# Kernel tuning notes

Measured on AMD Instinct MI355X. Metric: run time of the kernel, lower is better.

Reference implementation:

```python
import jax, jax.numpy as jnp
import numpy as np

ENC_IN, LAG = 14, 7
SEQ_LEN, PRED_LEN = 96, 96
NUM_SPLINE = 20
HID, LAYERS = 40, 2
F_RAW = ENC_IN + LAG - 1                 # 20 features into the CNN
F_CONV = F_RAW + 2 * 2 - (3 - 1) - 1 + 1 # 22 after Conv1d(k=3, pad=2)
F_CNN = (F_CONV + 2 * 1 - (3 - 1) - 1) // 2 + 1  # 11 after MaxPool1d(k=3, s=2, p=1)
B = 4096
T = SEQ_LEN + PRED_LEN                   # train_window = 192


def setup_inputs() -> dict:
    key = jax.random.key(0)
    ks = jax.random.split(key, 20)
    b0 = 0.02 * jax.random.normal(ks[10], (4 * HID,))
    b0 = b0.at[HID:2 * HID].add(2.0)  # forget-gate bias init (b_ih + b_hh = 1 + 1)
    b1 = 0.02 * jax.random.normal(ks[11], (4 * HID,))
    b1 = b1.at[HID:2 * HID].add(2.0)
    return {
        "x_enc": jax.random.normal(ks[0], (B, SEQ_LEN, ENC_IN + LAG), jnp.float32),
        "x_mark_enc": jax.random.normal(ks[1], (B, SEQ_LEN, 4), jnp.float32),
        "x_dec": jax.random.normal(ks[2], (B, PRED_LEN, 4), jnp.float32),
        "y_enc": jax.random.normal(ks[3], (B, PRED_LEN, ENC_IN + LAG), jnp.float32),
        "x_mark_dec": jax.random.normal(ks[4], (B, PRED_LEN, 4), jnp.float32),
        "conv_w": 0.3 * jax.random.normal(ks[5], (3,), jnp.float32),
        "conv_b": jnp.zeros((1,), jnp.float32),
        "bn_w": jnp.ones((), jnp.float32),
        "bn_b": jnp.zeros((), jnp.float32),
        "w_ih0": 0.15 * jax.random.normal(ks[6], (4 * HID, F_CNN), jnp.float32),
        "w_hh0": 0.15 * jax.random.normal(ks[7], (4 * HID, HID), jnp.float32),
        "b0": b0,
        "w_ih1": 0.15 * jax.random.normal(ks[8], (4 * HID, HID), jnp.float32),
        "w_hh1": 0.15 * jax.random.normal(ks[9], (4 * HID, HID), jnp.float32),
        "b1": b1,
        "w_gamma": 0.1 * jax.random.normal(ks[12], (1, LAYERS * HID), jnp.float32),
        "b_gamma": jnp.zeros((1,), jnp.float32),
        "w_eta": 0.1 * jax.random.normal(ks[13], (NUM_SPLINE, LAYERS * HID), jnp.float32),
        "b_eta": jnp.zeros((NUM_SPLINE,), jnp.float32),
    }


def _conv_block(x, conv_w, conv_b, bn_w, bn_b):
    # ConvLayer(1): Conv1d(1,1,k=3,pad=2,circular) + BatchNorm1d(1) + ELU + MaxPool1d(3,2,1)
    # x: [B, F_RAW] treated as (N=B, C=1, L=F_RAW)
    xp = jnp.pad(x, ((0, 0), (2, 2)), mode="wrap")
    y = conv_w[0] * xp[:, :-2] + conv_w[1] * xp[:, 1:-1] + conv_w[2] * xp[:, 2:] + conv_b  # [B, F_CONV]
    mu = y.mean()
    var = ((y - mu) ** 2).mean()  # training-mode BN, biased variance over (N, L)
    y = (y - mu) * jax.lax.rsqrt(var + 1e-5) * bn_w + bn_b
    y = jax.nn.elu(y)
    yp = jnp.pad(y, ((0, 0), (1, 1)), constant_values=-jnp.inf)
    idx = jnp.arange(F_CNN)[:, None] * 2 + jnp.arange(3)[None, :]  # [F_CNN, 3] window gather
    return yp[:, idx].max(axis=-1)  # [B, F_CNN]


def _cell(x, h, c, w_ih, w_hh, b):
    g = x @ w_ih.T + h @ w_hh.T + b
    i, f, gg, o = jnp.split(g, 4, axis=-1)  # torch gate order i,f,g,o
    c = jax.nn.sigmoid(f) * c + jax.nn.sigmoid(i) * jnp.tanh(gg)
    h = jax.nn.sigmoid(o) * jnp.tanh(c)
    return h, c


def reference(x_enc, x_mark_enc, x_dec, y_enc, x_mark_dec,
              conv_w, conv_b, bn_w, bn_b,
              w_ih0, w_hh0, b0, w_ih1, w_hh1, b1,
              w_gamma, b_gamma, w_eta, b_eta):
    batch = jnp.concatenate([x_enc, y_enc], axis=1)      # [B, T, D]
    train = batch[:, :, :-1].transpose(1, 0, 2)          # [T, B, F_RAW]
    nb = train.shape[1]
    init = (jnp.zeros((nb, HID)), jnp.zeros((nb, HID)),
            jnp.zeros((nb, HID)), jnp.zeros((nb, HID)))

    def step(carry, x_t):
        h0, c0, h1, c1 = carry
        feat = _conv_block(x_t, conv_w, conv_b, bn_w, bn_b)
        h0, c0 = _cell(feat, h0, c0, w_ih0, w_hh0, b0)
        h1, c1 = _cell(h0, h1, c1, w_ih1, w_hh1, b1)
        # hidden.permute(1,2,0).view(B,-1): interleave layers along last dim
        hp = jnp.stack([h0, h1], axis=-1).reshape(nb, LAYERS * HID)
        gamma = jax.nn.softplus(hp @ w_gamma.T + b_gamma)   # [B, 1]
        eta_k = jax.nn.softplus(hp @ w_eta.T + b_eta)       # [B, NUM_SPLINE]
        return (h0, c0, h1, c1), jnp.concatenate([gamma, eta_k], axis=-1)

    _, out = jax.lax.scan(step, init, train)
    return out  # [T, B, 1 + NUM_SPLINE]: per-step (gamma, eta_k) QSQM params of loss_list
```

## Files before the change

### kernel.cpp

```cpp
#include <hip/hip_runtime.h>
#include <cstdint>
#include <cstddef>

#define TSTEPS 192
#define BATCH  4096
#define FRAW   20
#define FCONV  22
#define FCNN   11
#define HID    40
#define NOUT   21
#define ROWSPB 16
#define NTH    768
#define NBLK   (BATCH/ROWSPB)

#define FEAT_OFF 4096

typedef _Float16 half8 __attribute__((ext_vector_type(8)));
typedef float    f32x4 __attribute__((ext_vector_type(4)));
#define MFMA16(a,b,c) __builtin_amdgcn_mfma_f32_16x16x32_f16(a,b,c,0,0,0)

#define WGBAR() do{ \
    __builtin_amdgcn_sched_barrier(0); \
    asm volatile("s_waitcnt lgkmcnt(0)" ::: "memory"); \
    __builtin_amdgcn_s_barrier(); \
    __builtin_amdgcn_sched_barrier(0); \
}while(0)

__device__ __forceinline__ float rcp_(float x){ return __builtin_amdgcn_rcpf(x); }
__device__ __forceinline__ float sigm_(float x){ return rcp_(1.f + __expf(-x)); }
__device__ __forceinline__ float tanh_(float x){ return fmaf(-2.f, rcp_(__expf(2.f*x) + 1.f), 1.f); }
__device__ __forceinline__ float softplus_(float x){
    float t = __expf(-fabsf(x));
    return fmaxf(x,0.f) + 0.6931471805599453f*__log2f(1.f+t);
}

__device__ __forceinline__ int offk(int k, int mr){
    return ((k>>5)*4 + ((k>>3)&3))*128 + mr*8 + (k&7);
}

__global__ __launch_bounds__(1024)
void statfeat_kernel(const float* __restrict__ x_enc, const float* __restrict__ y_enc,
                     const float* __restrict__ conv_w, const float* __restrict__ conv_b,
                     const float* __restrict__ bn_w, const float* __restrict__ bn_b,
                     _Float16* __restrict__ feat)
{
    const int t = blockIdx.x;
    const float w0=conv_w[0], w1=conv_w[1], w2=conv_w[2], cb=conv_b[0];
    const float* src = (t < 96) ? (x_enc + (size_t)t*21) : (y_enc + (size_t)(t-96)*21);

    float xv[4][FRAW];
    float s=0.f, ss=0.f;
    #pragma unroll
    for (int rr=0; rr<4; ++rr){
        const int row = threadIdx.x + 1024*rr;
        const float* xr = src + (size_t)row*2016;
        #pragma unroll
        for (int f=0; f<FRAW; ++f) xv[rr][f] = xr[f];
        #pragma unroll
        for (int i=0; i<FCONV; ++i){
            float y = fmaf(w0, xv[rr][(i+18)%20], fmaf(w1, xv[rr][(i+19)%20], fmaf(w2, xv[rr][i%20], cb)));
            s += y; ss = fmaf(y, y, ss);
        }
    }
    #pragma unroll
    for (int o=32; o>0; o>>=1){ s += __shfl_down(s,o); ss += __shfl_down(ss,o); }
    __shared__ float rs[16], rq[16], ab[2];
    const int wid = threadIdx.x >> 6, lid = threadIdx.x & 63;
    if (lid == 0){ rs[wid]=s; rq[wid]=ss; }
    __syncthreads();
    if (threadIdx.x == 0){
        float S=0.f, Q=0.f;
        #pragma unroll
        for (int i=0;i<16;++i){ S+=rs[i]; Q+=rq[i]; }
        const float N = (float)BATCH*(float)FCONV;
        float mu  = S/N;
        float var = Q/N - mu*mu;
        float A   = rsqrtf(var + 1e-5f) * bn_w[0];
        ab[0]=A; ab[1]=bn_b[0] - mu*A;
    }
    __syncthreads();
    const float A = ab[0], Bc = ab[1];

    #pragma unroll
    for (int rr=0; rr<4; ++rr){
        const int row = threadIdx.x + 1024*rr;
        float yv[FCONV];
        #pragma unroll
        for (int i=0; i<FCONV; ++i){
            float y = fmaf(w0, xv[rr][(i+18)%20], fmaf(w1, xv[rr][(i+19)%20], fmaf(w2, xv[rr][i%20], cb)));
            y = fmaf(y, A, Bc);
            yv[i] = (y > 0.f) ? y : (__expf(y) - 1.f);
        }
        _Float16* fo = feat + ((size_t)t*BATCH + row)*FCNN;
        #pragma unroll
        for (int i=0; i<FCNN; ++i){
            float m = (i==0) ? fmaxf(yv[0], yv[1])
                             : fmaxf(yv[2*i-1], fmaxf(yv[2*i], yv[2*i+1]));
            fo[i] = (_Float16)m;
        }
    }
}

__global__ __launch_bounds__(NTH, 3)
void lstm_kernel(const _Float16* __restrict__ feat,
                 const float* __restrict__ w_ih0, const float* __restrict__ w_hh0, const float* __restrict__ b0,
                 const float* __restrict__ w_ih1, const float* __restrict__ w_hh1, const float* __restrict__ b1,
                 const float* __restrict__ w_gamma, const float* __restrict__ b_gamma,
                 const float* __restrict__ w_eta,   const float* __restrict__ b_eta,
                 float* __restrict__ out)
{
    __shared__ __align__(16) _Float16 V[3*1536];

    const int tid  = threadIdx.x;
    const int l    = tid & 63;
    const int wv   = tid >> 6;
    const int q    = l >> 4;
    const int mr   = l & 15;
    const int row0 = blockIdx.x * ROWSPB;
    const bool isL0 = (wv < 5);
    const bool isL1 = (wv >= 5 && wv < 10);

    { uint32_t* z=(uint32_t*)V; for(int i=tid;i<2304;i+=NTH) z[i]=0u; }

    half8 a0h[2][2], a0l[2][2];
    half8 a1h[2][3], a1l[2][3];
    half8 ahd[3];
    f32x4 bias0[2]={{0,0,0,0},{0,0,0,0}}, bias1[2]={{0,0,0,0},{0,0,0,0}};
    f32x4 biash={0,0,0,0};
    int woH0[2]={0,0}, woH1[2]={0,0};
    int fW0=0, fW1=0; bool fV0=false, fV1=false;
    const _Float16* fG0 = feat; const _Float16* fG1 = feat;

    if (isL0){
        #pragma unroll
        for (int g=0; g<2; ++g){
            const int uA = 4*(2*wv+g) + (mr >> 2);
            const int RA = (mr & 3)*40 + uA;
            #pragma unroll
            for (int cc=0; cc<2; ++cc){
                #pragma unroll
                for (int ii=0; ii<8; ++ii){
                    int k = 32*cc + 8*q + ii;
                    float v = (k<11) ? w_ih0[RA*11+k] : ((k<51) ? w_hh0[RA*40+k-11] : 0.f);
                    _Float16 h = (_Float16)v;
                    a0h[g][cc][ii]=h; a0l[g][cc][ii]=(_Float16)(v-(float)h);
                }
            }
            const int u = 4*(2*wv+g) + q;
            bias0[g][0]=b0[u]; bias0[g][1]=b0[40+u]; bias0[g][2]=b0[80+u]; bias0[g][3]=b0[120+u];
            woH0[g] = offk(11+u, mr);
        }
    } else if (isL1){
        const int wl = wv - 5;
        #pragma unroll
        for (int g=0; g<2; ++g){
            const int uA = 4*(2*wl+g) + (mr >> 2);
            const int RA = (mr & 3)*40 + uA;
            #pragma unroll
            for (int cc=0; cc<3; ++cc){
                #pragma unroll
                for (int ii=0; ii<8; ++ii){
                    int k = 32*cc + 8*q + ii;
                    float v = 0.f;
                    if (k>=11 && k<51)      v = w_ih1[RA*40 + (k-11)];
                    else if (k>=56)         v = w_hh1[RA*40 + (k-56)];
                    _Float16 h = (_Float16)v;
                    a1h[g][cc][ii]=h; a1l[g][cc][ii]=(_Float16)(v-(float)h);
                }
            }
            const int u = 4*(2*wl+g) + q;
            bias1[g][0]=b1[u]; bias1[g][1]=b1[40+u]; bias1[g][2]=b1[80+u]; bias1[g][3]=b1[120+u];
            woH1[g] = offk(56+u, mr);
        }
    } else {
        const int hw = wv - 10;
        const int jo = 16*hw + mr;
        #pragma unroll
        for (int cc=0; cc<3; ++cc){
            #pragma unroll
            for (int ii=0; ii<8; ++ii){
                int k = 32*cc + 8*q + ii;
                float v = 0.f;
                if (jo < NOUT){
                    if (k>=11 && k<51) v = (jo==0) ? w_gamma[2*(k-11)]   : w_eta[(jo-1)*80 + 2*(k-11)];
                    else if (k>=56)    v = (jo==0) ? w_gamma[2*(k-56)+1] : w_eta[(jo-1)*80 + 2*(k-56)+1];
                }
                ahd[cc][ii] = (_Float16)v;
            }
        }
        #pragma unroll
        for (int e=0; e<4; ++e){
            int j2 = 16*hw + 4*q + e;
            biash[e] = (j2 < NOUT) ? ((j2==0) ? b_gamma[0] : b_eta[j2-1]) : 0.f;
        }
        const int hl = tid - 640;
        int i0 = hl, i1 = hl + 128;
        fV0 = (i0 < ROWSPB*FCNN); fV1 = (i1 < ROWSPB*FCNN);
        { int r = i0/FCNN, f = i0 - FCNN*r; r &= 15; fW0 = offk(f, r);
          fG0 = feat + (size_t)(row0 + r)*FCNN + f; }
        { int ix = fV1 ? i1 : 0;
          int r = ix/FCNN, f = ix - FCNN*(ix/FCNN); r &= 15; fW1 = offk(f, r);
          fG1 = feat + (size_t)(row0 + r)*FCNN + f; }
    }

    __syncthreads();
    _Float16 fA0=(_Float16)0.f, fA1=(_Float16)0.f, fB0=(_Float16)0.f, fB1=(_Float16)0.f;
    if (!isL0 && !isL1){
        if (fV0) V[fW0] = fG0[0];
        if (fV1) V[fW1] = fG1[0];
        const size_t fs = (size_t)BATCH*FCNN;
        if (fV0) fB0 = fG0[fs];
        if (fV1) fB1 = fG1[fs];
    }
    __syncthreads();

    float c0[2]={0.f,0.f}, c1[2]={0.f,0.f};
    const size_t featStep = (size_t)BATCH*FCNN;
    const _Float16* Vr = V + l*8;

    if (isL0){
        _Float16* wp0 = V + woH0[0];
        _Float16* wp1 = V + woH0[1];
        #define L0B(C,CN) do{ \
            half8 x0 = *(const half8*)(Vr + (C)*1536); \
            half8 x1 = *(const half8*)(Vr + (C)*1536 + 512); \
            { f32x4 acc = bias0[0]; \
              acc = MFMA16(a0h[0][0], x0, acc); \
              acc = MFMA16(a0l[0][0], x0, acc); \
              acc = MFMA16(a0h[0][1], x1, acc); \
              acc = MFMA16(a0l[0][1], x1, acc); \
              float ig=sigm_(acc[0]), fg=sigm_(acc[1]), gv=tanh_(acc[2]), og=sigm_(acc[3]); \
              c0[0] = fmaf(fg, c0[0], ig*gv); \
              wp0[(CN)*1536] = (_Float16)(og * tanh_(c0[0])); } \
            { f32x4 acc = bias0[1]; \
              acc = MFMA16(a0h[1][0], x0, acc); \
              acc = MFMA16(a0l[1][0], x0, acc); \
              acc = MFMA16(a0h[1][1], x1, acc); \
              acc = MFMA16(a0l[1][1], x1, acc); \
              float ig=sigm_(acc[0]), fg=sigm_(acc[1]), gv=tanh_(acc[2]), og=sigm_(acc[3]); \
              c0[1] = fmaf(fg, c0[1], ig*gv); \
              wp1[(CN)*1536] = (_Float16)(og * tanh_(c0[1])); } \
        }while(0)
        L0B(0,1); WGBAR();
        L0B(1,2); WGBAR();
        for (int m=0; m<32; ++m){
            #pragma unroll
            for (int k=0; k<6; ++k){
                const int i = 2 + 6*m + k;
                if (i < TSTEPS) L0B((k+2)%3, k%3);
                WGBAR();
            }
        }
        #undef L0B
    } else if (isL1){
        _Float16* wp0 = V + woH1[0];
        _Float16* wp1 = V + woH1[1];
        #define L1B(C,CN) do{ \
            half8 y0 = *(const half8*)(Vr + (C)*1536); \
            half8 y1 = *(const half8*)(Vr + (C)*1536 + 512); \
            half8 y2 = *(const half8*)(Vr + (C)*1536 + 1024); \
            { f32x4 cA = bias1[0]; \
              cA = MFMA16(a1h[0][0], y0, cA); cA = MFMA16(a1l[0][0], y0, cA); \
              cA = MFMA16(a1h[0][1], y1, cA); cA = MFMA16(a1l[0][1], y1, cA); \
              f32x4 cB = {0.f,0.f,0.f,0.f}; \
              cB = MFMA16(a1h[0][2], y2, cB); cB = MFMA16(a1l[0][2], y2, cB); \
              f32x4 acc = cA + cB; \
              float ig=sigm_(acc[0]), fg=sigm_(acc[1]), gv=tanh_(acc[2]), og=sigm_(acc[3]); \
              c1[0] = fmaf(fg, c1[0], ig*gv); \
              wp0[(CN)*1536] = (_Float16)(og * tanh_(c1[0])); } \
            { f32x4 cA = bias1[1]; \
              cA = MFMA16(a1h[1][0], y0, cA); cA = MFMA16(a1l[1][0], y0, cA); \
              cA = MFMA16(a1h[1][1], y1, cA); cA = MFMA16(a1l[1][1], y1, cA); \
              f32x4 cB = {0.f,0.f,0.f,0.f}; \
              cB = MFMA16(a1h[1][2], y2, cB); cB = MFMA16(a1l[1][2], y2, cB); \
              f32x4 acc = cA + cB; \
              float ig=sigm_(acc[0]), fg=sigm_(acc[1]), gv=tanh_(acc[2]), og=sigm_(acc[3]); \
              c1[1] = fmaf(fg, c1[1], ig*gv); \
              wp1[(CN)*1536] = (_Float16)(og * tanh_(c1[1])); } \
        }while(0)
        WGBAR();
        L1B(1,2); WGBAR();
        for (int m=0; m<32; ++m){
            #pragma unroll
            for (int k=0; k<6; ++k){
                const int i = 2 + 6*m + k;
                if (i <= TSTEPS) L1B((k+2)%3, k%3);
                WGBAR();
            }
        }
        #undef L1B
    } else {
        _Float16* fp0 = V + fW0;
        _Float16* fp1 = V + fW1;
        const int hw  = wv - 10;
        const int jb  = 16*hw + 4*q;
        float* outB = out + (size_t)(row0 + mr)*NOUT + jb;
        #define HFEAT(CN,PAR,I) do{ \
            if ((I) < TSTEPS-1){ \
                _Float16 v0 = (PAR) ? fA0 : fB0; \
                _Float16 v1 = (PAR) ? fA1 : fB1; \
                if (fV0) fp0[(CN)*1536] = v0; \
                if (fV1) fp1[(CN)*1536] = v1; \
            } \
            if ((I)+2 < TSTEPS){ \
                size_t o = (size_t)((I)+2)*featStep; \
                if (PAR){ if(fV0) fB0=fG0[o]; if(fV1) fB1=fG1[o]; } \
                else    { if(fV0) fA0=fG0[o]; if(fV1) fA1=fG1[o]; } \
            } \
        }while(0)
        #define HOUT(C,CP,I) do{ \
            half8 z0 = *(const half8*)(Vr + (CP)*1536); \
            half8 z1 = *(const half8*)(Vr + ((q<3)?(CP):(C))*1536 + 512); \
            half8 z2 = *(const half8*)(Vr + (C)*1536 + 1024); \
            f32x4 H = biash; \
            H = MFMA16(ahd[0], z0, H); \
            H = MFMA16(ahd[1], z1, H); \
            H = MFMA16(ahd[2], z2, H); \
            float* op = outB + (size_t)((I)-2)*(BATCH*NOUT); \
            if (hw==0 || q==0){ \
                op[0]=softplus_(H[0]); op[1]=softplus_(H[1]); \
                op[2]=softplus_(H[2]); op[3]=softplus_(H[3]); \
            } else if (q==1){ \
                op[0]=softplus_(H[0]); \
            } \
        }while(0)
        HFEAT(1,0,0); WGBAR();
        HFEAT(2,1,1); WGBAR();
        for (int m=0; m<32; ++m){
            #pragma unroll
            for (int k=0; k<6; ++k){
                const int i = 2 + 6*m + k;
                HFEAT(k%3, k%2, i);
                HOUT((k+2)%3, (k+1)%3, i);
                WGBAR();
            }
        }
        #undef HFEAT
        #undef HOUT
    }
}

extern "C" void kernel_launch(void* const* d_in, const int* in_sizes, int n_in,
                              void* d_out, int out_size, void* d_ws, size_t ws_size,
                              hipStream_t stream)
{
    (void)in_sizes; (void)n_in; (void)out_size; (void)ws_size;
    const float* x_enc   = (const float*)d_in[0];
    const float* y_enc   = (const float*)d_in[3];
    const float* conv_w  = (const float*)d_in[5];
    const float* conv_b  = (const float*)d_in[6];
    const float* bn_w    = (const float*)d_in[7];
    const float* bn_b    = (const float*)d_in[8];
    const float* w_ih0   = (const float*)d_in[9];
    const float* w_hh0   = (const float*)d_in[10];
    const float* b0      = (const float*)d_in[11];
    const float* w_ih1   = (const float*)d_in[12];
    const float* w_hh1   = (const float*)d_in[13];
    const float* b1      = (const float*)d_in[14];
    const float* w_gamma = (const float*)d_in[15];
    const float* b_gamma = (const float*)d_in[16];
    const float* w_eta   = (const float*)d_in[17];
    const float* b_eta   = (const float*)d_in[18];

    float*     out   = (float*)d_out;
    _Float16*  feat  = (_Float16*)((char*)d_ws + FEAT_OFF);

    statfeat_kernel<<<TSTEPS, 1024, 0, stream>>>(x_enc, y_enc, conv_w, conv_b, bn_w, bn_b, feat);
    lstm_kernel<<<NBLK, NTH, 0, stream>>>(feat,
        w_ih0, w_hh0, b0, w_ih1, w_hh1, b1, w_gamma, b_gamma, w_eta, b_eta, out);
}
```

Measured before the change: 170.7 us.

## Spread LSTM gate tiles across 16 waves with uneven per-wave tile counts

Raises the block from 12 to 16 waves. Layer-0 and layer-1 work now uses 7 waves each: 4 waves take one gate tile and 3 waves take two, where before 5 waves per layer each took two. The goal is a shorter per-step critical path in the barrier-synchronised recurrence. The cost is uneven load across waves, so the two-tile waves still set the step time, and possible register pressure or lower occupancy from the 1024-thread block with launch bound 4.

```diff
diff --git a/kernel.cpp b/kernel.cpp
--- a/kernel.cpp
+++ b/kernel.cpp
@@ -10,7 +10,7 @@
 #define HID    40
 #define NOUT   21
 #define ROWSPB 16
-#define NTH    768
+#define NTH    1024
 #define NBLK   (BATCH/ROWSPB)
 
 #define FEAT_OFF 4096
@@ -101,7 +101,7 @@
     }
 }
 
-__global__ __launch_bounds__(NTH, 3)
+__global__ __launch_bounds__(NTH, 4)
 void lstm_kernel(const _Float16* __restrict__ feat,
                  const float* __restrict__ w_ih0, const float* __restrict__ w_hh0, const float* __restrict__ b0,
                  const float* __restrict__ w_ih1, const float* __restrict__ w_hh1, const float* __restrict__ b1,
@@ -117,8 +117,15 @@
     const int q    = l >> 4;
     const int mr   = l & 15;
     const int row0 = blockIdx.x * ROWSPB;
-    const bool isL0 = (wv < 5);
-    const bool isL1 = (wv >= 5 && wv < 10);
+
+    int role, t0, ntl;
+    if      (wv < 4){  role=0; t0=wv;           ntl=1; }
+    else if (wv < 8){  role=1; t0=wv-4;         ntl=1; }
+    else if (wv < 11){ role=0; t0=4+2*(wv-8);   ntl=2; }
+    else if (wv < 14){ role=1; t0=4+2*(wv-11);  ntl=2; }
+    else            {  role=2; t0=0;            ntl=0; }
+    const bool isL0 = (role==0), isL1 = (role==1);
+    const bool two  = (ntl==2);
 
     { uint32_t* z=(uint32_t*)V; for(int i=tid;i<2304;i+=NTH) z[i]=0u; }
 
@@ -134,46 +141,51 @@
     if (isL0){
         #pragma unroll
         for (int g=0; g<2; ++g){
-            const int uA = 4*(2*wv+g) + (mr >> 2);
-            const int RA = (mr & 3)*40 + uA;
-            #pragma unroll
-            for (int cc=0; cc<2; ++cc){
+            if (g < ntl){
+                const int T  = t0 + g;
+                const int uA = 4*T + (mr >> 2);
+                const int RA = (mr & 3)*40 + uA;
                 #pragma unroll
-                for (int ii=0; ii<8; ++ii){
-                    int k = 32*cc + 8*q + ii;
-                    float v = (k<11) ? w_ih0[RA*11+k] : ((k<51) ? w_hh0[RA*40+k-11] : 0.f);
-                    _Float16 h = (_Float16)v;
-                    a0h[g][cc][ii]=h; a0l[g][cc][ii]=(_Float16)(v-(float)h);
+                for (int cc=0; cc<2; ++cc){
+                    #pragma unroll
+                    for (int ii=0; ii<8; ++ii){
+                        int k = 32*cc + 8*q + ii;
+                        float v = (k<11) ? w_ih0[RA*11+k] : ((k<51) ? w_hh0[RA*40+k-11] : 0.f);
+                        _Float16 h = (_Float16)v;
+                        a0h[g][cc][ii]=h; a0l[g][cc][ii]=(_Float16)(v-(float)h);
+                    }
                 }
-            }
-            const int u = 4*(2*wv+g) + q;
-            bias0[g][0]=b0[u]; bias0[g][1]=b0[40+u]; bias0[g][2]=b0[80+u]; bias0[g][3]=b0[120+u];
-            woH0[g] = offk(11+u, mr);
+                const int u = 4*T + q;
+                bias0[g][0]=b0[u]; bias0[g][1]=b0[40+u]; bias0[g][2]=b0[80+u]; bias0[g][3]=b0[120+u];
+                woH0[g] = offk(11+u, mr);
+            }
         }
     } else if (isL1){
-        const int wl = wv - 5;
         #pragma unroll
         for (int g=0; g<2; ++g){
-            const int uA = 4*(2*wl+g) + (mr >> 2);
-            const int RA = (mr & 3)*40 + uA;
-            #pragma unroll
-            for (int cc=0; cc<3; ++cc){
+            if (g < ntl){
+                const int T  = t0 + g;
+                const int uA = 4*T + (mr >> 2);
+                const int RA = (mr & 3)*40 + uA;
                 #pragma unroll
-                for (int ii=0; ii<8; ++ii){
-                    int k = 32*cc + 8*q + ii;
-                    float v = 0.f;
-                    if (k>=11 && k<51)      v = w_ih1[RA*40 + (k-11)];
-                    else if (k>=56)         v = w_hh1[RA*40 + (k-56)];
-                    _Float16 h = (_Float16)v;
-                    a1h[g][cc][ii]=h; a1l[g][cc][ii]=(_Float16)(v-(float)h);
+                for (int cc=0; cc<3; ++cc){
+                    #pragma unroll
+                    for (int ii=0; ii<8; ++ii){
+                        int k = 32*cc + 8*q + ii;
+                        float v = 0.f;
+                        if (k>=11 && k<51)      v = w_ih1[RA*40 + (k-11)];
+                        else if (k>=56)         v = w_hh1[RA*40 + (k-56)];
+                        _Float16 h = (_Float16)v;
+                        a1h[g][cc][ii]=h; a1l[g][cc][ii]=(_Float16)(v-(float)h);
+                    }
                 }
-            }
-            const int u = 4*(2*wl+g) + q;
-            bias1[g][0]=b1[u]; bias1[g][1]=b1[40+u]; bias1[g][2]=b1[80+u]; bias1[g][3]=b1[120+u];
-            woH1[g] = offk(56+u, mr);
+                const int u = 4*T + q;
+                bias1[g][0]=b1[u]; bias1[g][1]=b1[40+u]; bias1[g][2]=b1[80+u]; bias1[g][3]=b1[120+u];
+                woH1[g] = offk(56+u, mr);
+            }
         }
     } else {
-        const int hw = wv - 10;
+        const int hw = wv - 14;
         const int jo = 16*hw + mr;
         #pragma unroll
         for (int cc=0; cc<3; ++cc){
@@ -193,7 +205,7 @@
             int j2 = 16*hw + 4*q + e;
             biash[e] = (j2 < NOUT) ? ((j2==0) ? b_gamma[0] : b_eta[j2-1]) : 0.f;
         }
-        const int hl = tid - 640;
+        const int hl = tid - 896;
         int i0 = hl, i1 = hl + 128;
         fV0 = (i0 < ROWSPB*FCNN); fV1 = (i1 < ROWSPB*FCNN);
         { int r = i0/FCNN, f = i0 - FCNN*r; r &= 15; fW0 = offk(f, r);
@@ -205,7 +217,7 @@
 
     __syncthreads();
     _Float16 fA0=(_Float16)0.f, fA1=(_Float16)0.f, fB0=(_Float16)0.f, fB1=(_Float16)0.f;
-    if (!isL0 && !isL1){
+    if (role == 2){
         if (fV0) V[fW0] = fG0[0];
         if (fV1) V[fW1] = fG1[0];
         const size_t fs = (size_t)BATCH*FCNN;
@@ -219,27 +231,23 @@
     const _Float16* Vr = V + l*8;
 
     if (isL0){
-        _Float16* wp0 = V + woH0[0];
-        _Float16* wp1 = V + woH0[1];
+        _Float16* wpa = V + woH0[0];
+        _Float16* wpb = V + woH0[1];
+        #define L0T(G,WP,C,CN) do{ \
+            f32x4 acc = bias0[G]; \
+            acc = MFMA16(a0h[G][0], x0, acc); \
+            acc = MFMA16(a0l[G][0], x0, acc); \
+            acc = MFMA16(a0h[G][1], x1, acc); \
+            acc = MFMA16(a0l[G][1], x1, acc); \
+            float ig=sigm_(acc[0]), fg=sigm_(acc[1]), gv=tanh_(acc[2]), og=sigm_(acc[3]); \
+            c0[G] = fmaf(fg, c0[G], ig*gv); \
+            WP[(CN)*1536] = (_Float16)(og * tanh_(c0[G])); \
+        }while(0)
         #define L0B(C,CN) do{ \
             half8 x0 = *(const half8*)(Vr + (C)*1536); \
             half8 x1 = *(const half8*)(Vr + (C)*1536 + 512); \
-            { f32x4 acc = bias0[0]; \
-              acc = MFMA16(a0h[0][0], x0, acc); \
-              acc = MFMA16(a0l[0][0], x0, acc); \
-              acc = MFMA16(a0h[0][1], x1, acc); \
-              acc = MFMA16(a0l[0][1], x1, acc); \
-              float ig=sigm_(acc[0]), fg=sigm_(acc[1]), gv=tanh_(acc[2]), og=sigm_(acc[3]); \
-              c0[0] = fmaf(fg, c0[0], ig*gv); \
-              wp0[(CN)*1536] = (_Float16)(og * tanh_(c0[0])); } \
-            { f32x4 acc = bias0[1]; \
-              acc = MFMA16(a0h[1][0], x0, acc); \
-              acc = MFMA16(a0l[1][0], x0, acc); \
-              acc = MFMA16(a0h[1][1], x1, acc); \
-              acc = MFMA16(a0l[1][1], x1, acc); \
-              float ig=sigm_(acc[0]), fg=sigm_(acc[1]), gv=tanh_(acc[2]), og=sigm_(acc[3]); \
-              c0[1] = fmaf(fg, c0[1], ig*gv); \
-              wp1[(CN)*1536] = (_Float16)(og * tanh_(c0[1])); } \
+            L0T(0,wpa,C,CN); \
+            if (two) L0T(1,wpb,C,CN); \
         }while(0)
         L0B(0,1); WGBAR();
         L0B(1,2); WGBAR();
@@ -252,31 +260,27 @@
             }
         }
         #undef L0B
+        #undef L0T
     } else if (isL1){
-        _Float16* wp0 = V + woH1[0];
-        _Float16* wp1 = V + woH1[1];
+        _Float16* wpa = V + woH1[0];
+        _Float16* wpb = V + woH1[1];
+        #define L1T(G,WP,C,CN) do{ \
+            f32x4 cA = bias1[G]; \
+            cA = MFMA16(a1h[G][0], y0, cA); cA = MFMA16(a1l[G][0], y0, cA); \
+            cA = MFMA16(a1h[G][1], y1, cA); cA = MFMA16(a1l[G][1], y1, cA); \
+            f32x4 cB = {0.f,0.f,0.f,0.f}; \
+            cB = MFMA16(a1h[G][2], y2, cB); cB = MFMA16(a1l[G][2], y2, cB); \
+            f32x4 acc = cA + cB; \
+            float ig=sigm_(acc[0]), fg=sigm_(acc[1]), gv=tanh_(acc[2]), og=sigm_(acc[3]); \
+            c1[G] = fmaf(fg, c1[G], ig*gv); \
+            WP[(CN)*1536] = (_Float16)(og * tanh_(c1[G])); \
+        }while(0)
         #define L1B(C,CN) do{ \
             half8 y0 = *(const half8*)(Vr + (C)*1536); \
             half8 y1 = *(const half8*)(Vr + (C)*1536 + 512); \
             half8 y2 = *(const half8*)(Vr + (C)*1536 + 1024); \
-            { f32x4 cA = bias1[0]; \
-              cA = MFMA16(a1h[0][0], y0, cA); cA = MFMA16(a1l[0][0], y0, cA); \
-              cA = MFMA16(a1h[0][1], y1, cA); cA = MFMA16(a1l[0][1], y1, cA); \
-              f32x4 cB = {0.f,0.f,0.f,0.f}; \
-              cB = MFMA16(a1h[0][2], y2, cB); cB = MFMA16(a1l[0][2], y2, cB); \
-              f32x4 acc = cA + cB; \
-              float ig=sigm_(acc[0]), fg=sigm_(acc[1]), gv=tanh_(acc[2]), og=sigm_(acc[3]); \
-              c1[0] = fmaf(fg, c1[0], ig*gv); \
-              wp0[(CN)*1536] = (_Float16)(og * tanh_(c1[0])); } \
-            { f32x4 cA = bias1[1]; \
-              cA = MFMA16(a1h[1][0], y0, cA); cA = MFMA16(a1l[1][0], y0, cA); \
-              cA = MFMA16(a1h[1][1], y1, cA); cA = MFMA16(a1l[1][1], y1, cA); \
-              f32x4 cB = {0.f,0.f,0.f,0.f}; \
-              cB = MFMA16(a1h[1][2], y2, cB); cB = MFMA16(a1l[1][2], y2, cB); \
-              f32x4 acc = cA + cB; \
-              float ig=sigm_(acc[0]), fg=sigm_(acc[1]), gv=tanh_(acc[2]), og=sigm_(acc[3]); \
-              c1[1] = fmaf(fg, c1[1], ig*gv); \
-              wp1[(CN)*1536] = (_Float16)(og * tanh_(c1[1])); } \
+            L1T(0,wpa,C,CN); \
+            if (two) L1T(1,wpb,C,CN); \
         }while(0)
         WGBAR();
         L1B(1,2); WGBAR();
@@ -289,10 +293,11 @@
             }
         }
         #undef L1B
+        #undef L1T
     } else {
         _Float16* fp0 = V + fW0;
         _Float16* fp1 = V + fW1;
-        const int hw  = wv - 10;
+        const int hw  = wv - 14;
         const int jb  = 16*hw + 4*q;
         float* outB = out + (size_t)(row0 + mr)*NOUT + jb;
         #define HFEAT(CN,PAR,I) do{ \
```

After: 179.5 us. +5.1%, slower.
